# Kernel optimization log

Measured on AMD Instinct MI355X. Metric: run time of the kernel, lower is better.

Reference implementation:

```python
import jax, jax.numpy as jnp
import numpy as np
import math
from jax import lax

RNN = 256
N_MELS = 80
RF = 5
FRAME = N_MELS * RF  # 400
DYN_CH = 8
DYN_K = 21
STATIC_CH = 8
STATIC_K = 21
PRIOR_LEN = 11


def _betabinom_pmf(n, a, b):
    k = np.arange(n + 1, dtype=np.float64)
    lg = lambda x: np.array([math.lgamma(float(v)) for v in np.atleast_1d(x)])
    logC = lg(n + 1) - lg(k + 1) - lg(n - k + 1)
    logB = lg(k + a) + lg(n - k + b) - lg(np.full_like(k, n + a + b))
    logB0 = math.lgamma(a) + math.lgamma(b) - math.lgamma(a + b)
    return np.exp(logC + logB - logB0)

# prior buffer, flipped as in the torch module (register_buffer('P', ...flip(0)))
PRIOR = jnp.asarray(_betabinom_pmf(PRIOR_LEN - 1, 0.1, 0.9)[::-1].copy(), dtype=jnp.float32)


def gru_cell(x, h, wi, bi, wh, bh):
    # torch GRUCell math
    gi = x @ wi.T + bi
    gh = h @ wh.T + bh
    ir, iz, i_n = jnp.split(gi, 3, axis=-1)
    hr, hz, h_n = jnp.split(gh, 3, axis=-1)
    r = jax.nn.sigmoid(ir + hr)
    z = jax.nn.sigmoid(iz + hz)
    n = jnp.tanh(i_n + r * h_n)
    return (1.0 - z) * n + z * h


def dca(s, alpha, dW_w, dW_b, dV_w, dF_w, dU_w, dT_w, dT_b, dv_w):
    B, S = alpha.shape
    # betabinomial prior: causal conv with flipped pmf
    ap = jnp.pad(alpha, ((0, 0), (PRIOR_LEN - 1, 0)))[:, None, :]  # [B,1,S+10]
    p = lax.conv_general_dilated(ap, PRIOR.reshape(1, 1, -1), (1,), [(0, 0)],
                                 dimension_numbers=('NCH', 'OIH', 'NCH'))[:, 0]  # [B,S]
    p = jnp.log(jnp.clip(p, 1e-6))
    # dynamic filters: one set of 8 kernels per batch element
    G = jnp.tanh(s @ dW_w.T + dW_b) @ dV_w.T  # [B, 8*21]
    g = lax.conv_general_dilated(alpha[None, :, :], G.reshape(B * DYN_CH, 1, DYN_K),
                                 (1,), [((DYN_K - 1) // 2,) * 2],
                                 dimension_numbers=('NCH', 'OIH', 'NCH'),
                                 feature_group_count=B)  # [1, B*8, S]
    g = g.reshape(B, DYN_CH, S).transpose(0, 2, 1)  # [B,S,8]
    # static filters
    f = lax.conv_general_dilated(alpha[:, None, :], dF_w, (1,), [((STATIC_K - 1) // 2,) * 2],
                                 dimension_numbers=('NCH', 'OIH', 'NCH')).transpose(0, 2, 1)  # [B,S,8]
    e = (jnp.tanh(f @ dU_w.T + g @ dT_w.T + dT_b) @ dv_w.T)[..., 0] + p  # [B,S]
    return jax.nn.softmax(e, axis=-1)


def _decode(encoder_outputs, p1_w, p1_b, p2_w, p2_b, a_wi, a_bi, a_wh, a_bh,
            dW_w, dW_b, dV_w, dF_w, dU_w, dT_w, dT_b, dv_w, l_w, l_b,
            g1_wi, g1_bi, g1_wh, g1_bh, g2_wi, g2_bi, g2_wh, g2_bh, pr_w, pr_b, T_dec):
    B, S, _ = encoder_outputs.shape
    frame0 = jnp.zeros((B, FRAME), jnp.float32)
    alpha0 = jnp.zeros((B, S), jnp.float32).at[:, 0].set(1.0)
    ctx0 = jnp.zeros((B, 3 * RNN), jnp.float32)
    h0 = jnp.zeros((B, RNN), jnp.float32)

    def step(carry, _):
        frame, alpha, ctx, h_att, h1, h2 = carry
        # pre-net (eval mode: dropout is identity)
        pre = jax.nn.relu(jax.nn.relu(frame @ p1_w.T + p1_b) @ p2_w.T + p2_b)  # [B,128]
        h_att = gru_cell(jnp.concatenate([ctx, pre], axis=-1), h_att, a_wi, a_bi, a_wh, a_bh)
        alpha = dca(h_att, alpha, dW_w, dW_b, dV_w, dF_w, dU_w, dT_w, dT_b, dv_w)
        ctx = jnp.einsum('bs,bsd->bd', alpha, encoder_outputs)  # [B,768]
        x = jnp.concatenate([ctx, h_att], axis=-1) @ l_w.T + l_b  # [B,256]
        h1 = gru_cell(x, h1, g1_wi, g1_bi, g1_wh, g1_bh)
        x = x + h1
        h2 = gru_cell(x, h2, g2_wi, g2_bi, g2_wh, g2_bh)
        x = x + h2
        out = x @ pr_w.T + pr_b  # [B,400]
        return (out, alpha, ctx, h_att, h1, h2), out

    (_, alphaT, _, _, _, _), outs = lax.scan(step, (frame0, alpha0, ctx0, h0, h0, h0), None, length=T_dec)
    # outs: [T,B,400] -> [B,80,T*5]
    mel = outs.reshape(T_dec, B, N_MELS, RF).transpose(1, 2, 0, 3).reshape(B, N_MELS, T_dec * RF)
    return mel


def setup_inputs() -> dict:
    key = jax.random.key(0)
    ks = iter(jax.random.split(key, 40))
    w = lambda shape: jax.random.normal(next(ks), shape, jnp.float32) * 0.05
    z = lambda shape: jnp.zeros(shape, jnp.float32)
    B, S, D = 64, 512, 768
    return {
        'encoder_outputs': jax.random.normal(next(ks), (B, S, D), jnp.float32),
        'p1_w': w((RNN, FRAME)), 'p1_b': z((RNN,)),
        'p2_w': w((RNN // 2, RNN)), 'p2_b': z((RNN // 2,)),
        'a_wi': w((3 * RNN, 896)), 'a_bi': z((3 * RNN,)), 'a_wh': w((3 * RNN, RNN)), 'a_bh': z((3 * RNN,)),
        'dW_w': w((128, RNN)), 'dW_b': z((128,)),
        'dV_w': w((DYN_CH * DYN_K, 128)),
        'dF_w': w((STATIC_CH, 1, STATIC_K)),
        'dU_w': w((128, STATIC_CH)),
        'dT_w': w((128, DYN_CH)), 'dT_b': z((128,)),
        'dv_w': w((1, 128)),
        'l_w': w((RNN, 4 * RNN)), 'l_b': z((RNN,)),
        'g1_wi': w((3 * RNN, RNN)), 'g1_bi': z((3 * RNN,)), 'g1_wh': w((3 * RNN, RNN)), 'g1_bh': z((3 * RNN,)),
        'g2_wi': w((3 * RNN, RNN)), 'g2_bi': z((3 * RNN,)), 'g2_wh': w((3 * RNN, RNN)), 'g2_bh': z((3 * RNN,)),
        'pr_w': w((FRAME, RNN)), 'pr_b': z((FRAME,)),
        'T_dec': 250,
    }


def reference(encoder_outputs, p1_w, p1_b, p2_w, p2_b, a_wi, a_bi, a_wh, a_bh,
              dW_w, dW_b, dV_w, dF_w, dU_w, dT_w, dT_b, dv_w, l_w, l_b,
              g1_wi, g1_bi, g1_wh, g1_bh, g2_wi, g2_bi, g2_wh, g2_bh, pr_w, pr_b, T_dec):
    return _decode(encoder_outputs, p1_w, p1_b, p2_w, p2_b, a_wi, a_bi, a_wh, a_bh,
                   dW_w, dW_b, dV_w, dF_w, dU_w, dT_w, dT_b, dv_w, l_w, l_b,
                   g1_wi, g1_bi, g1_wh, g1_bh, g2_wi, g2_bi, g2_wh, g2_bh, pr_w, pr_b, T_dec)
```

## Files before the change

kernel.cpp:

```cpp
#include <hip/hip_runtime.h>
#include <cmath>

#define TDEC 250
#define EPS_A 1e-6f

#define NB_GRU1 64
#define NB_GRU2 96
#define NB_PROJ 128
#define NB_GIC  144
#define NB_GA   208
#define NBLK    224

#define B_CTX(p)  (8192   + (p)*49152)
#define B_HATT(p) (106496 + (p)*16384)
#define B_H1(p)   (139264 + (p)*16384)
#define B_H2(p)   (172032 + (p)*16384)
#define B_X(p)    (204800 + (p)*16384)
#define B_X2(p)   (237568 + (p)*16384)
#define B_X3(p)   (270336 + (p)*16384)
#define B_FR(p)   (303104 + (p)*25600)
#define B_GIC(p)  (354304 + (p)*49152)
#define B_GH(p)   (452608 + (p)*49152)
#define ZERO_END  550912
#define CVT_OFF   550912

#define OP1   0u
#define OP2   106496u
#define OAWI  139264u
#define OAWH  827392u
#define ODW   1024000u
#define OLW   1056768u
#define OG1I  1318912u
#define OG1H  1515520u
#define OG2I  1712128u
#define OG2H  1908736u
#define OPR   2105344u

struct Prior { float v[11]; };

struct KArgs {
  const float *enc;
  const float *p1w,*p1b,*p2w,*p2b;
  const float *awi,*abi,*awh,*abh;
  const float *dWw,*dWb,*dVw,*dFw,*dUw,*dTw,*dTb,*dvw;
  const float *lw,*lb;
  const float *g1wi,*g1bi,*g1wh,*g1bh;
  const float *g2wi,*g2bi,*g2wh,*g2bh;
  const float *prw,*prb;
  float* ws; float* dout;
  Prior pr;
};

__device__ __forceinline__ float gld(const float* p) {
  return __uint_as_float(__hip_atomic_load((const unsigned*)p, __ATOMIC_RELAXED, __HIP_MEMORY_SCOPE_AGENT));
}
__device__ __forceinline__ void gst(float* p, float v) {
  __hip_atomic_store((unsigned*)p, __float_as_uint(v), __ATOMIC_RELAXED, __HIP_MEMORY_SCOPE_AGENT);
}
__device__ __forceinline__ float sigm(float x) { return 1.f / (1.f + expf(-x)); }

__device__ __forceinline__ float dot8(uint4 w, float4 x0, float4 x1) {
  float a;
  a = __uint_as_float(w.x << 16) * x0.x;
  a = fmaf(__uint_as_float(w.x & 0xffff0000u), x0.y, a);
  a = fmaf(__uint_as_float(w.y << 16),         x0.z, a);
  a = fmaf(__uint_as_float(w.y & 0xffff0000u), x0.w, a);
  a = fmaf(__uint_as_float(w.z << 16),         x1.x, a);
  a = fmaf(__uint_as_float(w.z & 0xffff0000u), x1.y, a);
  a = fmaf(__uint_as_float(w.w << 16),         x1.z, a);
  a = fmaf(__uint_as_float(w.w & 0xffff0000u), x1.w, a);
  return a;
}

__global__ __launch_bounds__(256) void k_init(float* ws) {
  int idx = blockIdx.x * 256 + threadIdx.x;
  for (int i = idx; i < ZERO_END; i += gridDim.x * 256) ws[i] = 0.f;
}

struct CvtSeg { const float* src; unsigned dst; unsigned n; };
struct CvtArgs { CvtSeg s[11]; };
__global__ __launch_bounds__(256) void k_cvt(CvtArgs c, unsigned short* wb) {
  for (unsigned i = blockIdx.x * 256 + threadIdx.x; i < 256u * 416u; i += gridDim.x * 256) {
    unsigned row = i / 416u, col = i - row * 416u;
    unsigned short v = 0;
    if (col < 400u) {
      unsigned u = __float_as_uint(c.s[0].src[row * 400u + col]);
      v = (unsigned short)((u + 0x7fffu + ((u >> 16) & 1u)) >> 16);
    }
    wb[OP1 + i] = v;
  }
  for (int seg = 1; seg < 11; ++seg) {
    const float* s = c.s[seg].src;
    unsigned short* d = wb + c.s[seg].dst;
    unsigned n = c.s[seg].n;
    for (unsigned i = blockIdx.x * 256 + threadIdx.x; i < n; i += gridDim.x * 256) {
      unsigned u = __float_as_uint(s[i]);
      d[i] = (unsigned short)((u + 0x7fffu + ((u >> 16) & 1u)) >> 16);
    }
  }
}

__device__ __forceinline__ void postw(unsigned* fl, int word, unsigned v) {
  asm volatile("s_waitcnt vmcnt(0)" ::: "memory");
  __syncthreads();
  if (threadIdx.x == 0)
    __hip_atomic_store(&fl[blockIdx.x * 32 + word], v, __ATOMIC_RELAXED, __HIP_MEMORY_SCOPE_AGENT);
}
template <int SLP>
__device__ __forceinline__ void pollge(unsigned* fl, int line, int word, unsigned v) {
  while (__hip_atomic_load(&fl[line * 32 + word], __ATOMIC_RELAXED, __HIP_MEMORY_SCOPE_AGENT) < v)
    __builtin_amdgcn_s_sleep(SLP);
}

__device__ void gru_block(float* sm, unsigned* fl, float* ws, const unsigned short* wb,
                          int bg, int jg, int selfL0, int prodL0, int prodN, int prodWord,
                          unsigned OWh, unsigned OWi, const float* bi, const float* bh,
                          int offH0, int offXin0, int offXout0) {
  const int tid = threadIdx.x;
  const int B = bg * 16, J0 = jg * 32;
  float* hp   = sm;
  float* gh1l = sm + 4160;
  float* xs   = sm + 5696;
  float* gil  = sm + 9856;
  for (int t = 0; t < TDEC; ++t) {
    const int p = t & 1;
    if (tid < 8) pollge<4>(fl, selfL0 + tid, 0, (unsigned)t);
    __syncthreads();
    for (int idx = tid; idx < 4096; idx += 1024) {
      int bb = idx >> 8, k = idx & 255;
      hp[bb * 260 + k] = gld(ws + offH0 + (p ^ 1) * 16384 + (B + bb) * 256 + k);
    }
    __syncthreads();
#pragma unroll
    for (int pass = 0; pass < 2; ++pass) {
      if (tid < 768) {
        int lr = pass * 48 + (tid >> 4), bb = tid & 15;
        int wrow = (lr >> 5) * 256 + J0 + (lr & 31);
        const uint4* wr = (const uint4*)(wb + OWh + (size_t)wrow * 256);
        const float4* xr = (const float4*)(hp + bb * 260);
        float a = 0.f;
#pragma unroll 16
        for (int k4 = 0; k4 < 32; ++k4) a += dot8(wr[k4], xr[2*k4], xr[2*k4+1]);
        gh1l[lr * 16 + bb] = a + bh[wrow];
      }
    }
    if (tid < prodN) pollge<1>(fl, prodL0 + tid, prodWord, (unsigned)(t + 1));
    __syncthreads();
    for (int idx = tid; idx < 4096; idx += 1024) {
      int bb = idx >> 8, k = idx & 255;
      xs[bb * 260 + k] = gld(ws + offXin0 + p * 16384 + (B + bb) * 256 + k);
    }
    __syncthreads();
#pragma unroll
    for (int pass = 0; pass < 2; ++pass) {
      if (tid < 768) {
        int lr = pass * 48 + (tid >> 4), bb = tid & 15;
        int wrow = (lr >> 5) * 256 + J0 + (lr & 31);
        const uint4* wr = (const uint4*)(wb + OWi + (size_t)wrow * 256);
        const float4* xr = (const float4*)(xs + bb * 260);
        float a = 0.f;
#pragma unroll 16
        for (int k4 = 0; k4 < 32; ++k4) a += dot8(wr[k4], xr[2*k4], xr[2*k4+1]);
        gil[lr * 16 + bb] = a + bi[wrow];
      }
    }
    __syncthreads();
    if (tid < 512) {
      int lj = tid >> 4, bb = tid & 15;
      float r = sigm(gil[lj * 16 + bb] + gh1l[lj * 16 + bb]);
      float z = sigm(gil[(32 + lj) * 16 + bb] + gh1l[(32 + lj) * 16 + bb]);
      float n = tanhf(gil[(64 + lj) * 16 + bb] + r * gh1l[(64 + lj) * 16 + bb]);
      float hprev = hp[bb * 260 + J0 + lj];
      float hnew = (1.f - z) * n + z * hprev;
      gst(ws + offH0 + p * 16384 + (B + bb) * 256 + J0 + lj, hnew);
      gst(ws + offXout0 + p * 16384 + (B + bb) * 256 + J0 + lj, xs[bb * 260 + J0 + lj] + hnew);
    }
    postw(fl, 0, (unsigned)(t + 1));
  }
}

__global__ __launch_bounds__(1024, 1) void k_decode(KArgs A) {
  __shared__ __align__(16) float sm[31960];
  float* ws = A.ws;
  unsigned* fl = (unsigned*)ws;
  const unsigned short* wb = (const unsigned short*)(ws + CVT_OFF);
  const int blk = blockIdx.x;
  const int tid = threadIdx.x;

  if (blk < 64) {
    const int b = blk, bg = b >> 4;
    float* alpha = sm;
    float* hattl = sm + 512;
    float* sal   = sm + 768;
    float* fr    = sm + 1312;
    float* h1s   = sm + 1728;
    float* pre   = sm + 1984;
    float* sgi   = sm + 2112;
    float* sgh   = sm + 2880;
    float* t1    = sm + 3648;
    float* Gl    = sm + 3776;
    float* sdF   = sm + 3952;
    float* sdU   = sm + 4128;
    float* sdT   = sm + 5152;
    float* sdtb  = sm + 6176;
    float* sdv   = sm + 6304;
    float* es    = sm + 6432;
    float* e     = sm + 7456;
    float* red   = sm + 7968;
    int*   wc    = (int*)(sm + 7984);
    float* lv    = sm + 7992;
    short* li    = (short*)(sm + 8504);
    float* ctxl  = sm + 8760;
    float* sdV   = sm + 9528;

    if (tid < 512) alpha[tid] = (tid == 0) ? 1.f : 0.f;
    if (tid < 256) hattl[tid] = 0.f;
    if (tid < 176) sdF[tid] = (tid < 168) ? A.dFw[tid] : 0.f;
    if (tid >= 400 && tid < 416) fr[tid] = 0.f;
    sdU[tid] = A.dUw[tid];
    sdT[tid] = A.dTw[tid];
    if (tid < 128) { sdtb[tid] = A.dTb[tid]; sdv[tid] = A.dvw[tid]; }
    for (int i = tid; i < 21504; i += 1024) sdV[(i >> 7) * 132 + (i & 127)] = A.dVw[i];
    __syncthreads();

    for (int t = 0; t < TDEC; ++t) {
      const int p = t & 1;
      if (tid < 544) { int sg = tid - 10; sal[tid] = (sg >= 0 && sg < 512) ? alpha[sg] : 0.f; }
      else if (tid >= 544 && tid < 548) pollge<1>(fl, NB_PROJ + bg * 4 + (tid - 544), 0, (unsigned)t);
      __syncthreads();
      if (tid < 400) fr[tid] = gld(ws + B_FR(p) + b * 400 + tid);
      __syncthreads();
      {
        int j = tid >> 2, part = tid & 3;
        const uint4* wr = (const uint4*)(wb + OP1 + (size_t)j * 416) + part * 13;
        const float4* xr = (const float4*)fr + part * 26;
        float a = 0.f;
#pragma unroll
        for (int k4 = 0; k4 < 13; ++k4) a += dot8(wr[k4], xr[2*k4], xr[2*k4+1]);
        a += __shfl_xor(a, 1); a += __shfl_xor(a, 2);
        if (part == 0) h1s[j] = fmaxf(a + A.p1b[j], 0.f);
      }
      __syncthreads();
      {
        int j = tid >> 3, part = tid & 7;
        const uint4* wr = (const uint4*)(wb + OP2 + (size_t)j * 256) + part * 4;
        const float4* xr = (const float4*)h1s + part * 8;
        float a = 0.f;
#pragma unroll
        for (int k4 = 0; k4 < 4; ++k4) a += dot8(wr[k4], xr[2*k4], xr[2*k4+1]);
        a += __shfl_xor(a, 1); a += __shfl_xor(a, 2); a += __shfl_xor(a, 4);
        if (part == 0) pre[j] = fmaxf(a + A.p2b[j], 0.f);
      }
      __syncthreads();
      float gipre = 0.f;
      if (tid < 768) {
        const uint4* wr = (const uint4*)(wb + OAWI + (size_t)tid * 896 + 768);
        const float4* xr = (const float4*)pre;
        float a = 0.f;
#pragma unroll
        for (int k4 = 0; k4 < 16; ++k4) a += dot8(wr[k4], xr[2*k4], xr[2*k4+1]);
        gipre = a;
      } else if (tid < 784) {
        pollge<1>(fl, NB_GIC + bg * 16 + (tid - 768), 0, (unsigned)(t + 1));
      } else if (tid < 788) {
        pollge<1>(fl, NB_GA + bg * 4 + (tid - 784), 0, (unsigned)(t + 1));
      }
      __syncthreads();
      if (tid < 768) {
        sgi[tid] = gipre + gld(ws + B_GIC(p) + b * 768 + tid) + A.abi[tid];
        sgh[tid] = gld(ws + B_GH(p) + b * 768 + tid) + A.abh[tid];
      }
      __syncthreads();
      if (tid < 256) {
        float r = sigm(sgi[tid] + sgh[tid]);
        float z = sigm(sgi[256 + tid] + sgh[256 + tid]);
        float n = tanhf(sgi[512 + tid] + r * sgh[512 + tid]);
        float hnew = (1.f - z) * n + z * hattl[tid];
        hattl[tid] = hnew;
        gst(ws + B_HATT(p) + b * 256 + tid, hnew);
      }
      postw(fl, 1, (unsigned)(t + 1));
      {
        int j = tid >> 3, part = tid & 7;
        const uint4* wr = (const uint4*)(wb + ODW + (size_t)j * 256) + part * 4;
        const float4* xr = (const float4*)hattl + part * 8;
        float a = 0.f;
#pragma unroll
        for (int k4 = 0; k4 < 4; ++k4) a += dot8(wr[k4], xr[2*k4], xr[2*k4+1]);
        a += __shfl_xor(a, 1); a += __shfl_xor(a, 2); a += __shfl_xor(a, 4);
        if (part == 0) t1[j] = tanhf(a + A.dWb[j]);
      }
      __syncthreads();
      if (tid < 168) {
        const float4* wr = (const float4*)(sdV + tid * 132);
        const float4* xr = (const float4*)t1;
        float a = 0.f;
#pragma unroll 8
        for (int k4 = 0; k4 < 32; ++k4) {
          float4 av = xr[k4], wv = wr[k4];
          a = fmaf(av.x,wv.x, fmaf(av.y,wv.y, fmaf(av.z,wv.z, fmaf(av.w,wv.w, a))));
        }
        Gl[tid] = a;
      }
      __syncthreads();
      {
        int sl = tid >> 1, half = tid & 1;
        float f0[8], g0[8];
#pragma unroll
        for (int q = 0; q < 8; ++q) {
          float fa = 0.f, ga = 0.f;
#pragma unroll
          for (int k = 0; k < 21; ++k) {
            float a = sal[sl + k];
            fa = fmaf(sdF[q * 21 + k], a, fa);
            ga = fmaf(Gl[q * 21 + k], a, ga);
          }
          f0[q] = fa; g0[q] = ga;
        }
        float acc = 0.f;
        for (int cc = half * 64; cc < half * 64 + 64; ++cc) {
          float a = sdtb[cc];
#pragma unroll
          for (int q = 0; q < 8; ++q)
            a = fmaf(sdU[cc * 8 + q], f0[q], fmaf(sdT[cc * 8 + q], g0[q], a));
          acc = fmaf(sdv[cc], tanhf(a), acc);
        }
        es[sl * 2 + half] = acc;
      }
      __syncthreads();
      if (tid < 512) {
        float pr = 0.f;
#pragma unroll
        for (int k = 0; k < 11; ++k) pr = fmaf(A.pr.v[k], sal[tid + k], pr);
        e[tid] = es[tid * 2] + es[tid * 2 + 1] + logf(fmaxf(pr, 1e-6f));
      }
      __syncthreads();
      {
        int lane = tid & 63, wv = tid >> 6;
        float e0 = (tid < 512) ? e[tid] : -1e30f;
        float m = e0;
        for (int o = 32; o; o >>= 1) m = fmaxf(m, __shfl_xor(m, o));
        if (lane == 0) red[wv] = m;
        __syncthreads();
        m = red[0];
        for (int w = 1; w < 8; ++w) m = fmaxf(m, red[w]);
        float p0 = (tid < 512) ? expf(e0 - m) : 0.f;
        float s = p0;
        for (int o = 32; o; o >>= 1) s += __shfl_xor(s, o);
        __syncthreads();
        if (lane == 0) red[wv] = s;
        __syncthreads();
        float tot = red[0];
        for (int w = 1; w < 8; ++w) tot += red[w];
        float inv = 1.f / tot;
        float a0 = p0 * inv;
        if (tid < 512) alpha[tid] = a0;
        unsigned long long mk = __ballot(tid < 512 && a0 > EPS_A);
        if (lane == 0 && wv < 8) wc[wv] = (int)__popcll(mk);
        __syncthreads();
        int base = 0;
        for (int w = 0; w < wv && w < 8; ++w) base += wc[w];
        int n = 0;
        for (int w = 0; w < 8; ++w) n += wc[w];
        unsigned long long below = (1ull << lane) - 1ull;
        if (tid < 512 && a0 > EPS_A) {
          int pp = base + (int)__popcll(mk & below);
          li[pp] = (short)tid; lv[pp] = a0;
        }
        __syncthreads();
        const float* encb = A.enc + (size_t)b * 512 * 768;
        if (tid < 768) {
          float acc = 0.f;
          int i = 0;
          for (; i + 4 <= n; i += 4) {
            float v0 = gld(encb + (size_t)li[i] * 768 + tid);
            float v1 = gld(encb + (size_t)li[i+1] * 768 + tid);
            float v2 = gld(encb + (size_t)li[i+2] * 768 + tid);
            float v3 = gld(encb + (size_t)li[i+3] * 768 + tid);
            acc = fmaf(lv[i],v0, fmaf(lv[i+1],v1, fmaf(lv[i+2],v2, fmaf(lv[i+3],v3, acc))));
          }
          for (; i < n; ++i) acc = fmaf(lv[i], gld(encb + (size_t)li[i] * 768 + tid), acc);
          ctxl[tid] = acc;
          gst(ws + B_CTX(p) + b * 768 + tid, acc);
        }
      }
      postw(fl, 0, (unsigned)(t + 1));
      {
        int j = tid >> 2, part = tid & 3;
        const uint4* wr = (const uint4*)(wb + OLW + (size_t)j * 1024) + part * 32;
        const float4* xr = (part < 3) ? ((const float4*)ctxl + part * 64) : (const float4*)hattl;
        float a = 0.f;
#pragma unroll 16
        for (int k4 = 0; k4 < 32; ++k4) a += dot8(wr[k4], xr[2*k4], xr[2*k4+1]);
        a += __shfl_xor(a, 1); a += __shfl_xor(a, 2);
        if (part == 0) gst(ws + B_X(p) + b * 256 + j, a + A.lb[j]);
      }
      postw(fl, 2, (unsigned)(t + 1));
    }
  } else if (blk < NB_GRU2) {
    int rb = blk - NB_GRU1;
    int bg = rb >> 3, jg = rb & 7;
    gru_block(sm, fl, ws, wb, bg, jg, NB_GRU1 + bg * 8, bg * 16, 16, 2,
              OG1H, OG1I, A.g1bi, A.g1bh, B_H1(0), B_X(0), B_X2(0));
  } else if (blk < NB_PROJ) {
    int rb = blk - NB_GRU2;
    int bg = rb >> 3, jg = rb & 7;
    gru_block(sm, fl, ws, wb, bg, jg, NB_GRU2 + bg * 8, NB_GRU1 + bg * 8, 8, 0,
              OG2H, OG2I, A.g2bi, A.g2bh, B_H2(0), B_X2(0), B_X3(0));
  } else if (blk < NB_GIC) {
    int rb = blk - NB_PROJ, bg = rb >> 2, jg = rb & 3;
    int B = bg * 16, J0 = jg * 100;
    float* xs = sm;
    for (int t = 0; t < TDEC; ++t) {
      const int p = t & 1;
      if (tid < 8) pollge<1>(fl, NB_GRU2 + bg * 8 + tid, 0, (unsigned)(t + 1));
      __syncthreads();
      for (int idx = tid; idx < 4096; idx += 1024) {
        int bb = idx >> 8, k = idx & 255;
        xs[bb * 260 + k] = gld(ws + B_X3(p) + (B + bb) * 256 + k);
      }
      __syncthreads();
#pragma unroll
      for (int pass = 0; pass < 2; ++pass) {
        int bb = pass * 8 + (tid & 7), lj = tid >> 3;
        if (lj < 100) {
          int row = J0 + lj;
          const uint4* wr = (const uint4*)(wb + OPR + (size_t)row * 256);
          const float4* xr = (const float4*)(xs + bb * 260);
          float a = 0.f;
#pragma unroll 16
          for (int k4 = 0; k4 < 32; ++k4) a += dot8(wr[k4], xr[2*k4], xr[2*k4+1]);
          float v = a + A.prb[row];
          gst(ws + B_FR((t + 1) & 1) + (B + bb) * 400 + row, v);
          gst(A.dout + (size_t)(B + bb) * 100000 + (row / 5) * 1250 + t * 5 + (row % 5), v);
        }
      }
      postw(fl, 0, (unsigned)(t + 1));
    }
  } else if (blk < NB_GA) {
    int rb = blk - NB_GIC, bg = rb >> 4, jg = rb & 15;
    int B = bg * 16, R0 = jg * 48;
    float* cl = sm;
    for (int t = 0; t < TDEC; ++t) {
      const int p = t & 1;
      if (tid < 16) pollge<4>(fl, bg * 16 + tid, 0, (unsigned)t);
      __syncthreads();
      for (int idx = tid; idx < 12288; idx += 1024) {
        int bb = idx / 768, k = idx - bb * 768;
        cl[bb * 772 + k] = gld(ws + B_CTX(p ^ 1) + (B + bb) * 768 + k);
      }
      __syncthreads();
      if (tid < 768) {
        int rr = tid >> 4, bb = tid & 15;
        int row = R0 + rr;
        const uint4* wr = (const uint4*)(wb + OAWI + (size_t)row * 896);
        const float4* xr = (const float4*)(cl + bb * 772);
        float a = 0.f;
#pragma unroll 16
        for (int k4 = 0; k4 < 96; ++k4) a += dot8(wr[k4], xr[2*k4], xr[2*k4+1]);
        gst(ws + B_GIC(p) + (B + bb) * 768 + row, a);
      }
      postw(fl, 0, (unsigned)(t + 1));
    }
  } else {
    int rb = blk - NB_GA, bg = rb >> 2, jg = rb & 3;
    int B = bg * 16, R0 = jg * 192;
    float* hl = sm;
    for (int t = 0; t < TDEC; ++t) {
      const int p = t & 1;
      if (tid < 16) pollge<4>(fl, bg * 16 + tid, 1, (unsigned)t);
      __syncthreads();
      for (int idx = tid; idx < 4096; idx += 1024) {
        int bb = idx >> 8, k = idx & 255;
        hl[bb * 260 + k] = gld(ws + B_HATT(p ^ 1) + (B + bb) * 256 + k);
      }
      __syncthreads();
#pragma unroll
      for (int pass = 0; pass < 3; ++pass) {
        int rr = pass * 64 + (tid >> 4), bb = tid & 15;
        int row = R0 + rr;
        const uint4* wr = (const uint4*)(wb + OAWH + (size_t)row * 256);
        const float4* xr = (const float4*)(hl + bb * 260);
        float a = 0.f;
#pragma unroll 16
        for (int k4 = 0; k4 < 32; ++k4) a += dot8(wr[k4], xr[2*k4], xr[2*k4+1]);
        gst(ws + B_GH(p) + (B + bb) * 768 + row, a);
      }
      postw(fl, 0, (unsigned)(t + 1));
    }
  }
}

extern "C" void kernel_launch(void* const* d_in, const int* in_sizes, int n_in,
                              void* d_out, int out_size, void* d_ws, size_t ws_size,
                              hipStream_t stream) {
  (void)in_sizes; (void)n_in; (void)out_size; (void)ws_size;
  KArgs A;
  A.enc  = (const float*)d_in[0];
  A.p1w  = (const float*)d_in[1];  A.p1b  = (const float*)d_in[2];
  A.p2w  = (const float*)d_in[3];  A.p2b  = (const float*)d_in[4];
  A.awi  = (const float*)d_in[5];  A.abi  = (const float*)d_in[6];
  A.awh  = (const float*)d_in[7];  A.abh  = (const float*)d_in[8];
  A.dWw  = (const float*)d_in[9];  A.dWb  = (const float*)d_in[10];
  A.dVw  = (const float*)d_in[11]; A.dFw  = (const float*)d_in[12];
  A.dUw  = (const float*)d_in[13]; A.dTw  = (const float*)d_in[14];
  A.dTb  = (const float*)d_in[15]; A.dvw  = (const float*)d_in[16];
  A.lw   = (const float*)d_in[17]; A.lb   = (const float*)d_in[18];
  A.g1wi = (const float*)d_in[19]; A.g1bi = (const float*)d_in[20];
  A.g1wh = (const float*)d_in[21]; A.g1bh = (const float*)d_in[22];
  A.g2wi = (const float*)d_in[23]; A.g2bi = (const float*)d_in[24];
  A.g2wh = (const float*)d_in[25]; A.g2bh = (const float*)d_in[26];
  A.prw  = (const float*)d_in[27]; A.prb  = (const float*)d_in[28];
  A.ws   = (float*)d_ws;
  A.dout = (float*)d_out;

  {
    double aP = 0.1, bP = 0.9;
    double logB0 = lgamma(aP) + lgamma(bP) - lgamma(aP + bP);
    double pm[11];
    for (int k = 0; k <= 10; ++k) {
      double logC = lgamma(11.0) - lgamma(k + 1.0) - lgamma(11.0 - k);
      double logBt = lgamma(k + aP) + lgamma(10.0 - k + bP) - lgamma(10.0 + aP + bP);
      pm[k] = exp(logC + logBt - logB0);
    }
    for (int k = 0; k < 11; ++k) A.pr.v[k] = (float)pm[10 - k];
  }

  CvtArgs C;
  C.s[0]  = {A.p1w,  OP1,  106496u};
  C.s[1]  = {A.p2w,  OP2,  32768u};
  C.s[2]  = {A.awi,  OAWI, 688128u};
  C.s[3]  = {A.awh,  OAWH, 196608u};
  C.s[4]  = {A.dWw,  ODW,  32768u};
  C.s[5]  = {A.lw,   OLW,  262144u};
  C.s[6]  = {A.g1wi, OG1I, 196608u};
  C.s[7]  = {A.g1wh, OG1H, 196608u};
  C.s[8]  = {A.g2wi, OG2I, 196608u};
  C.s[9]  = {A.g2wh, OG2H, 196608u};
  C.s[10] = {A.prw,  OPR,  102400u};

  k_init<<<256, 256, 0, stream>>>((float*)d_ws);
  k_cvt<<<256, 256, 0, stream>>>(C, (unsigned short*)((float*)d_ws + CVT_OFF));
  k_decode<<<NBLK, 1024, 0, stream>>>(A);
}
```

Before: 33.18 ms.

## Fold decoder GRU input paths and projection into per-batch attention blocks

Moves the GRU1/GRU2 input-side matvecs, gate math and the frame projection into the 64 per-batch-element blocks, so each block computes them locally from shared memory. Only the hidden-side GRU matvecs stay on 16 dedicated blocks (8 per layer) that cover all 64 batch rows. This removes the global round-trips and flag handoffs for x, x2, x3 and the frame, and cuts the grid from 224 to 160 blocks. The dVw weights are now read as bf16 from the converted buffer instead of fp32 shared memory. The cost is a longer serial chain inside each batch block and possible bf16 rounding error in the dynamic filters.

```diff
diff --git a/kernel.cpp b/kernel.cpp
--- a/kernel.cpp
+++ b/kernel.cpp
@@ -4,37 +4,35 @@
 #define TDEC 250
 #define EPS_A 1e-6f
 
-#define NB_GRU1 64
-#define NB_GRU2 96
-#define NB_PROJ 128
-#define NB_GIC  144
-#define NB_GA   208
-#define NBLK    224
+#define NB_GIC  64
+#define NB_GA   128
+#define NB_WH1  144
+#define NB_WH2  152
+#define NBLK    160
 
 #define B_CTX(p)  (8192   + (p)*49152)
 #define B_HATT(p) (106496 + (p)*16384)
 #define B_H1(p)   (139264 + (p)*16384)
 #define B_H2(p)   (172032 + (p)*16384)
-#define B_X(p)    (204800 + (p)*16384)
-#define B_X2(p)   (237568 + (p)*16384)
-#define B_X3(p)   (270336 + (p)*16384)
-#define B_FR(p)   (303104 + (p)*25600)
-#define B_GIC(p)  (354304 + (p)*49152)
-#define B_GH(p)   (452608 + (p)*49152)
-#define ZERO_END  550912
-#define CVT_OFF   550912
+#define B_GIC(p)  (204800 + (p)*49152)
+#define B_GH(p)   (303104 + (p)*49152)
+#define B_GH1(p)  (401408 + (p)*49152)
+#define B_GH2(p)  (499712 + (p)*49152)
+#define ZERO_END  598016
+#define CVT_OFF   598016
 
 #define OP1   0u
 #define OP2   106496u
 #define OAWI  139264u
 #define OAWH  827392u
 #define ODW   1024000u
-#define OLW   1056768u
-#define OG1I  1318912u
-#define OG1H  1515520u
-#define OG2I  1712128u
-#define OG2H  1908736u
-#define OPR   2105344u
+#define ODV   1056768u
+#define OLW   1078272u
+#define OG1I  1340416u
+#define OG2I  1537024u
+#define OG1H  1733632u
+#define OG2H  1930240u
+#define OPR   2126848u
 
 struct Prior { float v[11]; };
 
@@ -78,7 +76,7 @@
 }
 
 struct CvtSeg { const float* src; unsigned dst; unsigned n; };
-struct CvtArgs { CvtSeg s[11]; };
+struct CvtArgs { CvtSeg s[12]; };
 __global__ __launch_bounds__(256) void k_cvt(CvtArgs c, unsigned short* wb) {
   for (unsigned i = blockIdx.x * 256 + threadIdx.x; i < 256u * 416u; i += gridDim.x * 256) {
     unsigned row = i / 416u, col = i - row * 416u;
@@ -89,7 +87,7 @@
     }
     wb[OP1 + i] = v;
   }
-  for (int seg = 1; seg < 11; ++seg) {
+  for (int seg = 1; seg < 12; ++seg) {
     const float* s = c.s[seg].src;
     unsigned short* d = wb + c.s[seg].dst;
     unsigned n = c.s[seg].n;
@@ -112,75 +110,8 @@
     __builtin_amdgcn_s_sleep(SLP);
 }
 
-__device__ void gru_block(float* sm, unsigned* fl, float* ws, const unsigned short* wb,
-                          int bg, int jg, int selfL0, int prodL0, int prodN, int prodWord,
-                          unsigned OWh, unsigned OWi, const float* bi, const float* bh,
-                          int offH0, int offXin0, int offXout0) {
-  const int tid = threadIdx.x;
-  const int B = bg * 16, J0 = jg * 32;
-  float* hp   = sm;
-  float* gh1l = sm + 4160;
-  float* xs   = sm + 5696;
-  float* gil  = sm + 9856;
-  for (int t = 0; t < TDEC; ++t) {
-    const int p = t & 1;
-    if (tid < 8) pollge<4>(fl, selfL0 + tid, 0, (unsigned)t);
-    __syncthreads();
-    for (int idx = tid; idx < 4096; idx += 1024) {
-      int bb = idx >> 8, k = idx & 255;
-      hp[bb * 260 + k] = gld(ws + offH0 + (p ^ 1) * 16384 + (B + bb) * 256 + k);
-    }
-    __syncthreads();
-#pragma unroll
-    for (int pass = 0; pass < 2; ++pass) {
-      if (tid < 768) {
-        int lr = pass * 48 + (tid >> 4), bb = tid & 15;
-        int wrow = (lr >> 5) * 256 + J0 + (lr & 31);
-        const uint4* wr = (const uint4*)(wb + OWh + (size_t)wrow * 256);
-        const float4* xr = (const float4*)(hp + bb * 260);
-        float a = 0.f;
-#pragma unroll 16
-        for (int k4 = 0; k4 < 32; ++k4) a += dot8(wr[k4], xr[2*k4], xr[2*k4+1]);
-        gh1l[lr * 16 + bb] = a + bh[wrow];
-      }
-    }
-    if (tid < prodN) pollge<1>(fl, prodL0 + tid, prodWord, (unsigned)(t + 1));
-    __syncthreads();
-    for (int idx = tid; idx < 4096; idx += 1024) {
-      int bb = idx >> 8, k = idx & 255;
-      xs[bb * 260 + k] = gld(ws + offXin0 + p * 16384 + (B + bb) * 256 + k);
-    }
-    __syncthreads();
-#pragma unroll
-    for (int pass = 0; pass < 2; ++pass) {
-      if (tid < 768) {
-        int lr = pass * 48 + (tid >> 4), bb = tid & 15;
-        int wrow = (lr >> 5) * 256 + J0 + (lr & 31);
-        const uint4* wr = (const uint4*)(wb + OWi + (size_t)wrow * 256);
-        const float4* xr = (const float4*)(xs + bb * 260);
-        float a = 0.f;
-#pragma unroll 16
-        for (int k4 = 0; k4 < 32; ++k4) a += dot8(wr[k4], xr[2*k4], xr[2*k4+1]);
-        gil[lr * 16 + bb] = a + bi[wrow];
-      }
-    }
-    __syncthreads();
-    if (tid < 512) {
-      int lj = tid >> 4, bb = tid & 15;
-      float r = sigm(gil[lj * 16 + bb] + gh1l[lj * 16 + bb]);
-      float z = sigm(gil[(32 + lj) * 16 + bb] + gh1l[(32 + lj) * 16 + bb]);
-      float n = tanhf(gil[(64 + lj) * 16 + bb] + r * gh1l[(64 + lj) * 16 + bb]);
-      float hprev = hp[bb * 260 + J0 + lj];
-      float hnew = (1.f - z) * n + z * hprev;
-      gst(ws + offH0 + p * 16384 + (B + bb) * 256 + J0 + lj, hnew);
-      gst(ws + offXout0 + p * 16384 + (B + bb) * 256 + J0 + lj, xs[bb * 260 + J0 + lj] + hnew);
-    }
-    postw(fl, 0, (unsigned)(t + 1));
-  }
-}
-
 __global__ __launch_bounds__(1024, 1) void k_decode(KArgs A) {
-  __shared__ __align__(16) float sm[31960];
+  __shared__ __align__(16) float sm[16640];
   float* ws = A.ws;
   unsigned* fl = (unsigned*)ws;
   const unsigned short* wb = (const unsigned short*)(ws + CVT_OFF);
@@ -191,44 +122,44 @@
     const int b = blk, bg = b >> 4;
     float* alpha = sm;
     float* hattl = sm + 512;
-    float* sal   = sm + 768;
-    float* fr    = sm + 1312;
-    float* h1s   = sm + 1728;
-    float* pre   = sm + 1984;
-    float* sgi   = sm + 2112;
-    float* sgh   = sm + 2880;
-    float* t1    = sm + 3648;
-    float* Gl    = sm + 3776;
-    float* sdF   = sm + 3952;
-    float* sdU   = sm + 4128;
-    float* sdT   = sm + 5152;
-    float* sdtb  = sm + 6176;
-    float* sdv   = sm + 6304;
-    float* es    = sm + 6432;
-    float* e     = sm + 7456;
-    float* red   = sm + 7968;
-    int*   wc    = (int*)(sm + 7984);
-    float* lv    = sm + 7992;
-    short* li    = (short*)(sm + 8504);
-    float* ctxl  = sm + 8760;
-    float* sdV   = sm + 9528;
+    float* h1l   = sm + 768;
+    float* h2l   = sm + 1024;
+    float* fr    = sm + 1280;
+    float* ctxl  = sm + 1696;
+    float* xl    = sm + 2464;
+    float* x2l   = sm + 2720;
+    float* x3l   = sm + 2976;
+    float* sal   = sm + 3232;
+    float* h1s   = sm + 3776;
+    float* pre   = sm + 4032;
+    float* sgi   = sm + 4160;
+    float* sgh   = sm + 4928;
+    float* t1    = sm + 5696;
+    float* Gl    = sm + 5824;
+    float* sdF   = sm + 6000;
+    float* sdU   = sm + 6176;
+    float* sdT   = sm + 7200;
+    float* sdtb  = sm + 8224;
+    float* sdv   = sm + 8352;
+    float* es    = sm + 8480;
+    float* e     = sm + 9504;
+    float* red   = sm + 10016;
+    int*   wc    = (int*)(sm + 10032);
+    float* lv    = sm + 10040;
+    short* li    = (short*)(sm + 10552);
 
     if (tid < 512) alpha[tid] = (tid == 0) ? 1.f : 0.f;
-    if (tid < 256) hattl[tid] = 0.f;
+    if (tid < 256) { hattl[tid] = 0.f; h1l[tid] = 0.f; h2l[tid] = 0.f; }
+    if (tid < 416) fr[tid] = 0.f;
     if (tid < 176) sdF[tid] = (tid < 168) ? A.dFw[tid] : 0.f;
-    if (tid >= 400 && tid < 416) fr[tid] = 0.f;
     sdU[tid] = A.dUw[tid];
     sdT[tid] = A.dTw[tid];
     if (tid < 128) { sdtb[tid] = A.dTb[tid]; sdv[tid] = A.dvw[tid]; }
-    for (int i = tid; i < 21504; i += 1024) sdV[(i >> 7) * 132 + (i & 127)] = A.dVw[i];
     __syncthreads();
 
     for (int t = 0; t < TDEC; ++t) {
       const int p = t & 1;
       if (tid < 544) { int sg = tid - 10; sal[tid] = (sg >= 0 && sg < 512) ? alpha[sg] : 0.f; }
-      else if (tid >= 544 && tid < 548) pollge<1>(fl, NB_PROJ + bg * 4 + (tid - 544), 0, (unsigned)t);
-      __syncthreads();
-      if (tid < 400) fr[tid] = gld(ws + B_FR(p) + b * 400 + tid);
       __syncthreads();
       {
         int j = tid >> 2, part = tid & 3;
@@ -292,14 +223,11 @@
       }
       __syncthreads();
       if (tid < 168) {
-        const float4* wr = (const float4*)(sdV + tid * 132);
+        const uint4* wr = (const uint4*)(wb + ODV + (size_t)tid * 128);
         const float4* xr = (const float4*)t1;
         float a = 0.f;
-#pragma unroll 8
-        for (int k4 = 0; k4 < 32; ++k4) {
-          float4 av = xr[k4], wv = wr[k4];
-          a = fmaf(av.x,wv.x, fmaf(av.y,wv.y, fmaf(av.z,wv.z, fmaf(av.w,wv.w, a))));
-        }
+#pragma unroll
+        for (int k4 = 0; k4 < 16; ++k4) a += dot8(wr[k4], xr[2*k4], xr[2*k4+1]);
         Gl[tid] = a;
       }
       __syncthreads();
@@ -393,49 +321,82 @@
 #pragma unroll 16
         for (int k4 = 0; k4 < 32; ++k4) a += dot8(wr[k4], xr[2*k4], xr[2*k4+1]);
         a += __shfl_xor(a, 1); a += __shfl_xor(a, 2);
-        if (part == 0) gst(ws + B_X(p) + b * 256 + j, a + A.lb[j]);
-      }
-      postw(fl, 2, (unsigned)(t + 1));
-    }
-  } else if (blk < NB_GRU2) {
-    int rb = blk - NB_GRU1;
-    int bg = rb >> 3, jg = rb & 7;
-    gru_block(sm, fl, ws, wb, bg, jg, NB_GRU1 + bg * 8, bg * 16, 16, 2,
-              OG1H, OG1I, A.g1bi, A.g1bh, B_H1(0), B_X(0), B_X2(0));
-  } else if (blk < NB_PROJ) {
-    int rb = blk - NB_GRU2;
-    int bg = rb >> 3, jg = rb & 7;
-    gru_block(sm, fl, ws, wb, bg, jg, NB_GRU2 + bg * 8, NB_GRU1 + bg * 8, 8, 0,
-              OG2H, OG2I, A.g2bi, A.g2bh, B_H2(0), B_X2(0), B_X3(0));
-  } else if (blk < NB_GIC) {
-    int rb = blk - NB_PROJ, bg = rb >> 2, jg = rb & 3;
-    int B = bg * 16, J0 = jg * 100;
-    float* xs = sm;
-    for (int t = 0; t < TDEC; ++t) {
-      const int p = t & 1;
-      if (tid < 8) pollge<1>(fl, NB_GRU2 + bg * 8 + tid, 0, (unsigned)(t + 1));
-      __syncthreads();
-      for (int idx = tid; idx < 4096; idx += 1024) {
-        int bb = idx >> 8, k = idx & 255;
-        xs[bb * 260 + k] = gld(ws + B_X3(p) + (B + bb) * 256 + k);
-      }
-      __syncthreads();
-#pragma unroll
-      for (int pass = 0; pass < 2; ++pass) {
-        int bb = pass * 8 + (tid & 7), lj = tid >> 3;
-        if (lj < 100) {
-          int row = J0 + lj;
-          const uint4* wr = (const uint4*)(wb + OPR + (size_t)row * 256);
-          const float4* xr = (const float4*)(xs + bb * 260);
+        if (part == 0) xl[j] = a + A.lb[j];
+      }
+      __syncthreads();
+      {
+        float giv = 0.f;
+        if (tid < 768) {
+          const uint4* wr = (const uint4*)(wb + OG1I + (size_t)tid * 256);
+          const float4* xr = (const float4*)xl;
           float a = 0.f;
 #pragma unroll 16
           for (int k4 = 0; k4 < 32; ++k4) a += dot8(wr[k4], xr[2*k4], xr[2*k4+1]);
-          float v = a + A.prb[row];
-          gst(ws + B_FR((t + 1) & 1) + (B + bb) * 400 + row, v);
-          gst(A.dout + (size_t)(B + bb) * 100000 + (row / 5) * 1250 + t * 5 + (row % 5), v);
-        }
-      }
-      postw(fl, 0, (unsigned)(t + 1));
+          giv = a;
+        } else if (tid < 776) {
+          pollge<1>(fl, NB_WH1 + (tid - 768), 0, (unsigned)(t + 1));
+        }
+        __syncthreads();
+        if (tid < 768) {
+          sgi[tid] = giv + A.g1bi[tid];
+          sgh[tid] = gld(ws + B_GH1(p) + b * 768 + tid);
+        }
+        __syncthreads();
+        if (tid < 256) {
+          float r = sigm(sgi[tid] + sgh[tid]);
+          float z = sigm(sgi[256 + tid] + sgh[256 + tid]);
+          float n = tanhf(sgi[512 + tid] + r * sgh[512 + tid]);
+          float hnew = (1.f - z) * n + z * h1l[tid];
+          h1l[tid] = hnew;
+          gst(ws + B_H1(p) + b * 256 + tid, hnew);
+          x2l[tid] = xl[tid] + hnew;
+        }
+        postw(fl, 2, (unsigned)(t + 1));
+      }
+      {
+        float giv = 0.f;
+        if (tid < 768) {
+          const uint4* wr = (const uint4*)(wb + OG2I + (size_t)tid * 256);
+          const float4* xr = (const float4*)x2l;
+          float a = 0.f;
+#pragma unroll 16
+          for (int k4 = 0; k4 < 32; ++k4) a += dot8(wr[k4], xr[2*k4], xr[2*k4+1]);
+          giv = a;
+        } else if (tid < 776) {
+          pollge<1>(fl, NB_WH2 + (tid - 768), 0, (unsigned)(t + 1));
+        }
+        __syncthreads();
+        if (tid < 768) {
+          sgi[tid] = giv + A.g2bi[tid];
+          sgh[tid] = gld(ws + B_GH2(p) + b * 768 + tid);
+        }
+        __syncthreads();
+        if (tid < 256) {
+          float r = sigm(sgi[tid] + sgh[tid]);
+          float z = sigm(sgi[256 + tid] + sgh[256 + tid]);
+          float n = tanhf(sgi[512 + tid] + r * sgh[512 + tid]);
+          float hnew = (1.f - z) * n + z * h2l[tid];
+          h2l[tid] = hnew;
+          gst(ws + B_H2(p) + b * 256 + tid, hnew);
+          x3l[tid] = x2l[tid] + hnew;
+        }
+        postw(fl, 3, (unsigned)(t + 1));
+      }
+      if (tid < 800) {
+        int j = tid >> 1, part = tid & 1;
+        const uint4* wr = (const uint4*)(wb + OPR + (size_t)j * 256) + part * 16;
+        const float4* xr = (const float4*)x3l + part * 32;
+        float a = 0.f;
+#pragma unroll 16
+        for (int k4 = 0; k4 < 16; ++k4) a += dot8(wr[k4], xr[2*k4], xr[2*k4+1]);
+        a += __shfl_xor(a, 1);
+        if (part == 0) {
+          float v = a + A.prb[j];
+          fr[j] = v;
+          gst(A.dout + (size_t)b * 100000 + (j / 5) * 1250 + t * 5 + (j % 5), v);
+        }
+      }
+      __syncthreads();
     }
   } else if (blk < NB_GA) {
     int rb = blk - NB_GIC, bg = rb >> 4, jg = rb & 15;
@@ -462,7 +423,7 @@
       }
       postw(fl, 0, (unsigned)(t + 1));
     }
-  } else {
+  } else if (blk < NB_WH1) {
     int rb = blk - NB_GA, bg = rb >> 2, jg = rb & 3;
     int B = bg * 16, R0 = jg * 192;
     float* hl = sm;
@@ -485,6 +446,39 @@
 #pragma unroll 16
         for (int k4 = 0; k4 < 32; ++k4) a += dot8(wr[k4], xr[2*k4], xr[2*k4+1]);
         gst(ws + B_GH(p) + (B + bb) * 768 + row, a);
+      }
+      postw(fl, 0, (unsigned)(t + 1));
+    }
+  } else {
+    const int isW2 = (blk >= NB_WH2);
+    const int w = blk - (isW2 ? NB_WH2 : NB_WH1);
+    const unsigned OW = isW2 ? OG2H : OG1H;
+    const float* bh = isW2 ? A.g2bh : A.g1bh;
+    const int hOff0  = isW2 ? B_H2(0)  : B_H1(0);
+    const int ghOff0 = isW2 ? B_GH2(0) : B_GH1(0);
+    const int word = isW2 ? 3 : 2;
+    const int R0 = w * 96;
+    float* hl = sm;
+    for (int t = 0; t < TDEC; ++t) {
+      const int p = t & 1;
+      if (tid < 64) pollge<4>(fl, tid, word, (unsigned)t);
+      __syncthreads();
+      for (int idx = tid; idx < 16384; idx += 1024) {
+        int bb = idx >> 8, k = idx & 255;
+        hl[bb * 260 + k] = gld(ws + hOff0 + (p ^ 1) * 16384 + bb * 256 + k);
+      }
+      __syncthreads();
+#pragma unroll
+      for (int pass = 0; pass < 6; ++pass) {
+        int o = pass * 1024 + tid;
+        int bb = o & 63, lr = o >> 6;
+        int row = R0 + lr;
+        const uint4* wr = (const uint4*)(wb + OW + (size_t)row * 256);
+        const float4* xr = (const float4*)(hl + bb * 260);
+        float a = 0.f;
+#pragma unroll 16
+        for (int k4 = 0; k4 < 32; ++k4) a += dot8(wr[k4], xr[2*k4], xr[2*k4+1]);
+        gst(ws + ghOff0 + p * 49152 + bb * 768 + row, a + bh[row]);
       }
       postw(fl, 0, (unsigned)(t + 1));
     }
@@ -532,12 +526,13 @@
   C.s[2]  = {A.awi,  OAWI, 688128u};
   C.s[3]  = {A.awh,  OAWH, 196608u};
   C.s[4]  = {A.dWw,  ODW,  32768u};
-  C.s[5]  = {A.lw,   OLW,  262144u};
-  C.s[6]  = {A.g1wi, OG1I, 196608u};
-  C.s[7]  = {A.g1wh, OG1H, 196608u};
+  C.s[5]  = {A.dVw,  ODV,  21504u};
+  C.s[6]  = {A.lw,   OLW,  262144u};
+  C.s[7]  = {A.g1wi, OG1I, 196608u};
   C.s[8]  = {A.g2wi, OG2I, 196608u};
-  C.s[9]  = {A.g2wh, OG2H, 196608u};
-  C.s[10] = {A.prw,  OPR,  102400u};
+  C.s[9]  = {A.g1wh, OG1H, 196608u};
+  C.s[10] = {A.g2wh, OG2H, 196608u};
+  C.s[11] = {A.prw,  OPR,  102400u};
 
   k_init<<<256, 256, 0, stream>>>((float*)d_ws);
   k_cvt<<<256, 256, 0, stream>>>(C, (unsigned short*)((float*)d_ws + CVT_OFF));
```

New measurement: 34.81 ms. 4.9% more time.
